# Kernel tuning notes

Measured on AMD Instinct MI355X. Metric: run time of the kernel, lower is better.

Reference implementation:

```python
import jax, jax.numpy as jnp
import numpy as np

BN_EPS = 1e-5
ATT_EPS = 1e-6


def _conv(x, w, groups=1):
    # x: [B,C,H,W], w: [O, C//groups, k, k], stride 1, SAME padding for odd k
    k = w.shape[-1]
    p = (k - 1) // 2
    return jax.lax.conv_general_dilated(
        x, w, window_strides=(1, 1), padding=[(p, p), (p, p)],
        dimension_numbers=('NCHW', 'OIHW', 'NCHW'), feature_group_count=groups)


def _bn(x, bnp):
    # bnp: [4, C] stacked (scale, bias, running_mean, running_var); eval-mode BN
    s, b, m, v = bnp[0], bnp[1], bnp[2], bnp[3]
    inv = s / jnp.sqrt(v + BN_EPS)
    return x * inv[None, :, None, None] + (b - m * inv)[None, :, None, None]


def _relu6(x):
    return jnp.clip(x, 0.0, 6.0)


def _ffn(x, fc1_w, fc1_bn, conv1_w, conv1_bn, conv2_w, conv2_bn, fc2_w, fc2_bn):
    # E_FFN: 1x1 ConvBNReLU6 -> dw5x5 ConvBNReLU6 & dw3x3 ConvBNReLU6 -> sum -> 1x1 ConvBN -> ReLU6
    C = x.shape[1]
    h = _relu6(_bn(_conv(x, fc1_w), fc1_bn))
    x1 = _relu6(_bn(_conv(h, conv1_w, groups=C), conv1_bn))
    x2 = _relu6(_bn(_conv(h, conv2_w, groups=C), conv2_bn))
    return _relu6(_bn(_conv(x1 + x2, fc2_w), fc2_bn))


def _bias(y, b):
    return y + b[None, :, None, None]


def setup_inputs() -> dict:
    key = jax.random.key(0)
    ks = jax.random.split(key, 16)
    C, M = 64, 8  # in_places, in_places // scale
    B, H, W = 4, 224, 224

    def w(k, shape, s=0.05):
        return (jax.random.normal(k, shape, dtype=jnp.float32) * s)

    def bn_params(k, c):
        k1, k2, k3, k4 = jax.random.split(k, 4)
        scale = 1.0 + 0.1 * jax.random.normal(k1, (c,), dtype=jnp.float32)
        bias = 0.1 * jax.random.normal(k2, (c,), dtype=jnp.float32)
        mean = 0.1 * jax.random.normal(k3, (c,), dtype=jnp.float32)
        var = 1.0 + 0.1 * jax.random.uniform(k4, (c,), dtype=jnp.float32)
        return jnp.stack([scale, bias, mean, var])  # [4, c]

    return {
        'x': jax.random.normal(ks[0], (B, C, H, W), dtype=jnp.float32),
        'gamma': jnp.full((1,), 0.5, dtype=jnp.float32),  # nonzero so attention branch matters
        'q_w': w(ks[1], (M, C, 1, 1)), 'q_b': w(ks[2], (M,)),
        'k_w': w(ks[3], (M, C, 1, 1)), 'k_b': w(ks[4], (M,)),
        'v_w': w(ks[5], (C, C, 1, 1)), 'v_b': w(ks[6], (C,)),
        'fc1_w': w(ks[7], (C, C, 1, 1)), 'fc1_bn': bn_params(ks[8], C),
        'conv1_w': w(ks[9], (C, 1, 5, 5)), 'conv1_bn': bn_params(ks[10], C),
        'conv2_w': w(ks[11], (C, 1, 3, 3)), 'conv2_bn': bn_params(ks[12], C),
        'fc2_w': w(ks[13], (C, C, 1, 1)), 'fc2_bn': bn_params(ks[14], C),
    }


def reference(x, gamma, q_w, q_b, k_w, k_b, v_w, v_b,
              fc1_w, fc1_bn, conv1_w, conv1_bn, conv2_w, conv2_bn, fc2_w, fc2_bn):
    B, C, H, W = x.shape
    N = H * W
    x_channel = _ffn(x, fc1_w, fc1_bn, conv1_w, conv1_bn, conv2_w, conv2_bn, fc2_w, fc2_bn)
    # softplus feature maps; Q,K: [B, m, N]
    Q = jax.nn.softplus(_bias(_conv(x, q_w), q_b).reshape(B, -1, N))
    K = jax.nn.softplus(_bias(_conv(x, k_w), k_b).reshape(B, -1, N))
    V = (_bias(_conv(x, v_w), v_b) + x_channel).reshape(B, C, N)
    Qt = jnp.swapaxes(Q, 1, 2)                              # [B, N, m]
    KV = jnp.einsum('bmn,bcn->bmc', K, V)                   # [B, m, C]
    norm = 1.0 / jnp.einsum('bnm,bm->bn', Qt, K.sum(-1) + ATT_EPS)  # [B, N]
    wv = jnp.einsum('bnm,bmc,bn->bcn', Qt, KV, norm).reshape(B, C, H, W)
    return x + gamma * wv
```

## Files before the change

kernel.cpp:

```cpp
#include <hip/hip_runtime.h>
#include <math.h>

#define B_ 4
#define C_ 64
#define M_ 8
#define H_ 224
#define W_ 224
#define N_ (H_*W_)
#define CN_ (C_*N_)
#define MN_ (M_*N_)
#define BCN_ (B_*CN_)
#define BMN_ (B_*MN_)

__device__ __forceinline__ float relu6f(float v){ return fminf(fmaxf(v,0.0f),6.0f); }
__device__ __forceinline__ float softplusf(float v){
  return v > 0.0f ? v + log1pf(expf(-v)) : log1pf(expf(v));
}

#define FMA4(A, W, X) { A.x = fmaf((W), (X).x, A.x); A.y = fmaf((W), (X).y, A.y); \
                        A.z = fmaf((W), (X).z, A.z); A.w = fmaf((W), (X).w, A.w); }

__global__ __launch_bounds__(256) void k_fc1k(const float* __restrict__ x,
                                              const float* __restrict__ w,
                                              const float* __restrict__ bn,
                                              const float* __restrict__ kw,
                                              const float* __restrict__ kb,
                                              float* __restrict__ h,
                                              float* __restrict__ Kq)
{
  __shared__ float xsl[2*1024];
  __shared__ float wl [2*512];
  __shared__ float kt [512];
  const int tid  = threadIdx.x;
  const int b    = blockIdx.x / 392;
  const int pg   = blockIdx.x % 392;
  const int pix0 = pg*128;
  const float* xb = x + (size_t)b*CN_ + pix0;

  for (int idx = tid; idx < 512; idx += 256) {
    const int c = idx >> 3, m = idx & 7;
    kt[idx] = kw[m*64 + c];
  }

  const int scp = tid >> 5;
  const int spx = (tid & 31) << 2;
  const int e0 = tid*2, e1 = tid*2+1;
  const int wc0 = e0 >> 6, wo0 = e0 & 63;
  const int wc1 = e1 >> 6, wo1 = e1 & 63;

  {
    const float4 xr = *(const float4*)(xb + (size_t)scp*N_ + spx);
    const float w0r = w[wo0*64 + wc0];
    const float w1r = w[wo1*64 + wc1];
    *(float4*)&xsl[scp*128 + spx] = xr;
    wl[e0] = w0r; wl[e1] = w1r;
  }
  __syncthreads();

  const int lane = tid & 63, wv_ = tid >> 6;
  const int och  = 2*wv_ + (lane >> 5);
  const int ocb  = och*8;
  const int px4  = (lane & 31) << 2;

  float4 ah[8];
  float4 ak = {0,0,0,0};
  #pragma unroll
  for (int i = 0; i < 8; ++i) ah[i] = make_float4(0.f,0.f,0.f,0.f);

  for (int ck = 0; ck < 8; ++ck) {
    const int cur = ck & 1, nxt = cur ^ 1;
    const float* xc = &xsl[cur*1024];
    const float* wc = &wl[cur*512];
    float4 xr; float w0r, w1r;
    if (ck < 7) {
      const int c0n = (ck+1)*8;
      xr  = *(const float4*)(xb + (size_t)(c0n + scp)*N_ + spx);
      w0r = w[wo0*64 + c0n + wc0];
      w1r = w[wo1*64 + c0n + wc1];
    }
    #pragma unroll
    for (int cp = 0; cp < 8; ++cp) {
      const float4 xv = *(const float4*)&xc[cp*128 + px4];
      const float4 w0 = *(const float4*)&wc[cp*64 + ocb];
      const float4 w1 = *(const float4*)&wc[cp*64 + ocb + 4];
      const float kvw = kt[(ck*8+cp)*8 + och];
      FMA4(ah[0], w0.x, xv); FMA4(ah[1], w0.y, xv);
      FMA4(ah[2], w0.z, xv); FMA4(ah[3], w0.w, xv);
      FMA4(ah[4], w1.x, xv); FMA4(ah[5], w1.y, xv);
      FMA4(ah[6], w1.z, xv); FMA4(ah[7], w1.w, xv);
      FMA4(ak, kvw, xv);
    }
    if (ck < 7) {
      *(float4*)&xsl[nxt*1024 + scp*128 + spx] = xr;
      wl[nxt*512 + e0] = w0r; wl[nxt*512 + e1] = w1r;
    }
    __syncthreads();
  }

  float* hb = h + (size_t)b*CN_ + pix0 + px4;
  #pragma unroll
  for (int o = 0; o < 8; ++o) {
    const int oc = ocb + o;
    const float inv  = bn[oc] / sqrtf(bn[192+oc] + 1e-5f);
    const float beta = bn[64+oc] - bn[128+oc]*inv;
    float4 o4;
    o4.x = relu6f(fmaf(ah[o].x, inv, beta));
    o4.y = relu6f(fmaf(ah[o].y, inv, beta));
    o4.z = relu6f(fmaf(ah[o].z, inv, beta));
    o4.w = relu6f(fmaf(ah[o].w, inv, beta));
    *(float4*)(hb + (size_t)oc*N_) = o4;
  }
  {
    const float kbm = kb[och];
    float4 q;
    q.x = softplusf(ak.x + kbm); q.y = softplusf(ak.y + kbm);
    q.z = softplusf(ak.z + kbm); q.w = softplusf(ak.w + kbm);
    *(float4*)(Kq + (size_t)b*MN_ + (size_t)och*N_ + pix0 + px4) = q;
  }
}

__global__ __launch_bounds__(256) void k_dw(const float* __restrict__ h,
                                            const float* __restrict__ w5,
                                            const float* __restrict__ w3,
                                            const float* __restrict__ bn1,
                                            const float* __restrict__ bn2,
                                            float* __restrict__ s)
{
  __shared__ float tile[36*37];
  const int tid = threadIdx.x;
  const int blk = blockIdx.x;
  const int t   = blk % 49;
  const int bc  = blk / 49;
  const int c   = bc & 63;
  const int tx0 = (t % 7) * 32;
  const int ty0 = (t / 7) * 32;
  const float* hb = h + (size_t)bc * N_;

  for (int idx = tid; idx < 1296; idx += 256) {
    const int ly = idx / 36, lx = idx - ly*36;
    const int gy = ty0 + ly - 2, gx = tx0 + lx - 2;
    float v = 0.0f;
    if (gy >= 0 && gy < H_ && gx >= 0 && gx < W_) v = hb[gy*W_ + gx];
    tile[ly*37 + lx] = v;
  }
  __syncthreads();

  float w5r[25], w3r[9];
  #pragma unroll
  for (int i = 0; i < 25; ++i) w5r[i] = w5[c*25 + i];
  #pragma unroll
  for (int i = 0; i < 9; ++i)  w3r[i] = w3[c*9 + i];
  const float inv1 = bn1[c] / sqrtf(bn1[192+c] + 1e-5f);
  const float bet1 = bn1[64+c] - bn1[128+c]*inv1;
  const float inv2 = bn2[c] / sqrtf(bn2[192+c] + 1e-5f);
  const float bet2 = bn2[64+c] - bn2[128+c]*inv2;

  const int ty  = tid >> 3;
  const int tx4 = (tid & 7) << 2;
  float a5[4] = {0,0,0,0}, a3[4] = {0,0,0,0};
  #pragma unroll
  for (int dy = 0; dy < 5; ++dy) {
    float r[8];
    #pragma unroll
    for (int i = 0; i < 8; ++i) r[i] = tile[(ty+dy)*37 + tx4 + i];
    #pragma unroll
    for (int dx = 0; dx < 5; ++dx) {
      const float wv = w5r[dy*5+dx];
      #pragma unroll
      for (int p = 0; p < 4; ++p) a5[p] = fmaf(wv, r[p+dx], a5[p]);
    }
    if (dy >= 1 && dy <= 3) {
      #pragma unroll
      for (int dx = 1; dx <= 3; ++dx) {
        const float wv = w3r[(dy-1)*3+(dx-1)];
        #pragma unroll
        for (int p = 0; p < 4; ++p) a3[p] = fmaf(wv, r[p+dx], a3[p]);
      }
    }
  }
  float* sb = s + (size_t)bc * N_ + (ty0+ty)*W_ + tx0 + tx4;
  float4 o4;
  o4.x = relu6f(fmaf(a5[0],inv1,bet1)) + relu6f(fmaf(a3[0],inv2,bet2));
  o4.y = relu6f(fmaf(a5[1],inv1,bet1)) + relu6f(fmaf(a3[1],inv2,bet2));
  o4.z = relu6f(fmaf(a5[2],inv1,bet1)) + relu6f(fmaf(a3[2],inv2,bet2));
  o4.w = relu6f(fmaf(a5[3],inv1,bet1)) + relu6f(fmaf(a3[3],inv2,bet2));
  *(float4*)sb = o4;
}

__global__ __launch_bounds__(256) void k_v(const float* __restrict__ x,
                                           const float* __restrict__ s,
                                           const float* __restrict__ vw,
                                           const float* __restrict__ vb,
                                           const float* __restrict__ fw,
                                           const float* __restrict__ fbn,
                                           float* __restrict__ V)
{
  __shared__ float xsl[2*1024];
  __shared__ float ssl[2*1024];
  __shared__ float wvl[2*512];
  __shared__ float wfl[2*512];
  const int tid  = threadIdx.x;
  const int b    = blockIdx.x / 392;
  const int pg   = blockIdx.x % 392;
  const int pix0 = pg*128;
  const float* xb = x + (size_t)b*CN_ + pix0;
  const float* sb = s + (size_t)b*CN_ + pix0;

  const int scp = tid >> 5;
  const int spx = (tid & 31) << 2;
  const int e0 = tid*2, e1 = tid*2+1;
  const int wc0 = e0 >> 6, wo0 = e0 & 63;
  const int wc1 = e1 >> 6, wo1 = e1 & 63;

  {
    const float4 xr = *(const float4*)(xb + (size_t)scp*N_ + spx);
    const float4 sr = *(const float4*)(sb + (size_t)scp*N_ + spx);
    const float a0 = vw[wo0*64 + wc0], a1 = vw[wo1*64 + wc1];
    const float f0 = fw[wo0*64 + wc0], f1 = fw[wo1*64 + wc1];
    *(float4*)&xsl[scp*128 + spx] = xr;
    *(float4*)&ssl[scp*128 + spx] = sr;
    wvl[e0] = a0; wvl[e1] = a1;
    wfl[e0] = f0; wfl[e1] = f1;
  }
  __syncthreads();

  const int lane = tid & 63, wv_ = tid >> 6;
  const int och  = 2*wv_ + (lane >> 5);
  const int ocb  = och*8;
  const int px4  = (lane & 31) << 2;

  float4 av[8], af[8];
  #pragma unroll
  for (int i = 0; i < 8; ++i) { av[i] = make_float4(0,0,0,0); af[i] = make_float4(0,0,0,0); }

  for (int ck = 0; ck < 8; ++ck) {
    const int cur = ck & 1, nxt = cur ^ 1;
    const float* xc = &xsl[cur*1024];
    const float* sc2 = &ssl[cur*1024];
    const float* wvc = &wvl[cur*512];
    const float* wfc = &wfl[cur*512];
    float4 xr, sr; float a0r, a1r, f0r, f1r;
    if (ck < 7) {
      const int c0n = (ck+1)*8;
      xr  = *(const float4*)(xb + (size_t)(c0n + scp)*N_ + spx);
      sr  = *(const float4*)(sb + (size_t)(c0n + scp)*N_ + spx);
      a0r = vw[wo0*64 + c0n + wc0]; a1r = vw[wo1*64 + c0n + wc1];
      f0r = fw[wo0*64 + c0n + wc0]; f1r = fw[wo1*64 + c0n + wc1];
    }
    #pragma unroll
    for (int cp = 0; cp < 8; ++cp) {
      const float4 xv = *(const float4*)&xc[cp*128 + px4];
      const float4 sv = *(const float4*)&sc2[cp*128 + px4];
      const float4 wa0 = *(const float4*)&wvc[cp*64 + ocb];
      const float4 wa1 = *(const float4*)&wvc[cp*64 + ocb + 4];
      const float4 wf0 = *(const float4*)&wfc[cp*64 + ocb];
      const float4 wf1 = *(const float4*)&wfc[cp*64 + ocb + 4];
      FMA4(av[0], wa0.x, xv); FMA4(av[1], wa0.y, xv);
      FMA4(av[2], wa0.z, xv); FMA4(av[3], wa0.w, xv);
      FMA4(av[4], wa1.x, xv); FMA4(av[5], wa1.y, xv);
      FMA4(av[6], wa1.z, xv); FMA4(av[7], wa1.w, xv);
      FMA4(af[0], wf0.x, sv); FMA4(af[1], wf0.y, sv);
      FMA4(af[2], wf0.z, sv); FMA4(af[3], wf0.w, sv);
      FMA4(af[4], wf1.x, sv); FMA4(af[5], wf1.y, sv);
      FMA4(af[6], wf1.z, sv); FMA4(af[7], wf1.w, sv);
    }
    if (ck < 7) {
      *(float4*)&xsl[nxt*1024 + scp*128 + spx] = xr;
      *(float4*)&ssl[nxt*1024 + scp*128 + spx] = sr;
      wvl[nxt*512 + e0] = a0r; wvl[nxt*512 + e1] = a1r;
      wfl[nxt*512 + e0] = f0r; wfl[nxt*512 + e1] = f1r;
    }
    __syncthreads();
  }

  float* Vb = V + (size_t)b*CN_ + pix0 + px4;
  #pragma unroll
  for (int o = 0; o < 8; ++o) {
    const int oc = ocb + o;
    const float inv  = fbn[oc] / sqrtf(fbn[192+oc] + 1e-5f);
    const float beta = fbn[64+oc] - fbn[128+oc]*inv;
    const float bias = vb[oc];
    float4 o4;
    o4.x = av[o].x + bias + relu6f(fmaf(af[o].x, inv, beta));
    o4.y = av[o].y + bias + relu6f(fmaf(af[o].y, inv, beta));
    o4.z = av[o].z + bias + relu6f(fmaf(af[o].z, inv, beta));
    o4.w = av[o].w + bias + relu6f(fmaf(af[o].w, inv, beta));
    *(float4*)(Vb + (size_t)oc*N_) = o4;
  }
}

__global__ __launch_bounds__(256) void k_kv(const float* __restrict__ V,
                                            const float* __restrict__ Kq,
                                            float* __restrict__ KV,
                                            float* __restrict__ Ksum)
{
  const int blk = blockIdx.x;
  const int b   = blk >> 7;
  const int rem = blk & 127;
  const int cg  = rem >> 4;
  const int ch  = rem & 15;
  const int tid = threadIdx.x;
  const int base = ch * 3136;
  const int end  = base + 3136;
  const float* Kb = Kq + (size_t)b*MN_;
  const float* Vb = V  + (size_t)b*CN_ + (size_t)(cg*8)*N_;

  float acc[64];
  #pragma unroll
  for (int i = 0; i < 64; ++i) acc[i] = 0.0f;
  float ks[8] = {0,0,0,0,0,0,0,0};

  for (int n = base + tid; n < end; n += 256) {
    float kv[8];
    #pragma unroll
    for (int m2 = 0; m2 < 8; ++m2) kv[m2] = Kb[m2*N_ + n];
    #pragma unroll
    for (int m2 = 0; m2 < 8; ++m2) ks[m2] += kv[m2];
    #pragma unroll
    for (int c8 = 0; c8 < 8; ++c8) {
      const float vv = Vb[c8*N_ + n];
      #pragma unroll
      for (int m2 = 0; m2 < 8; ++m2)
        acc[m2*8+c8] = fmaf(kv[m2], vv, acc[m2*8+c8]);
    }
  }
  const int lane = tid & 63;
  float mine = 0.0f;
  #pragma unroll
  for (int jj = 0; jj < 64; ++jj) {
    float v = acc[jj];
    v += __shfl_xor(v, 1);
    v += __shfl_xor(v, 2);
    v += __shfl_xor(v, 4);
    v += __shfl_xor(v, 8);
    v += __shfl_xor(v, 16);
    v += __shfl_xor(v, 32);
    if (lane == jj) mine = v;
  }
  atomicAdd(&KV[b*512 + (lane>>3)*64 + cg*8 + (lane&7)], mine);
  if (cg == 0) {
    float mk = 0.0f;
    #pragma unroll
    for (int jj = 0; jj < 8; ++jj) {
      float v = ks[jj];
      v += __shfl_xor(v, 1);
      v += __shfl_xor(v, 2);
      v += __shfl_xor(v, 4);
      v += __shfl_xor(v, 8);
      v += __shfl_xor(v, 16);
      v += __shfl_xor(v, 32);
      if (lane == jj) mk = v;
    }
    if (lane < 8) atomicAdd(&Ksum[b*8 + lane], mk);
  }
}

__global__ __launch_bounds__(256) void k_out(const float* __restrict__ x,
                                             const float* __restrict__ qw,
                                             const float* __restrict__ qb,
                                             const float* __restrict__ gamma,
                                             const float* __restrict__ KV,
                                             const float* __restrict__ Ksum,
                                             float* __restrict__ out)
{
  __shared__ float xs[64*256];
  __shared__ __align__(16) float kvt[64*8];
  __shared__ __align__(16) float wqt[64*8];
  __shared__ float ksl[8];
  const int tid = threadIdx.x;
  const int b  = blockIdx.x / 196;
  const int pg = blockIdx.x % 196;
  const int pix0 = pg*256;
  const float* xb = x + (size_t)b*CN_ + pix0;

  for (int idx = tid; idx < 512; idx += 256) {
    const int m = idx >> 6, c = idx & 63;
    kvt[c*8 + m] = KV[b*512 + idx];
    wqt[c*8 + m] = qw[idx];
  }
  if (tid < 8) ksl[tid] = Ksum[b*8 + tid] + 1e-6f;
  for (int idx = tid; idx < 4096; idx += 256) {
    const int c = idx >> 6, i = idx & 63;
    const float4 v = ((const float4*)(xb + (size_t)c*N_))[i];
    ((float4*)&xs[c*256])[i] = v;
  }
  __syncthreads();

  float q[8] = {0,0,0,0,0,0,0,0};
  #pragma unroll 8
  for (int c = 0; c < 64; ++c) {
    const float xv = xs[c*256 + tid];
    const float4 w0 = *(const float4*)&wqt[c*8];
    const float4 w1 = *(const float4*)&wqt[c*8+4];
    q[0] = fmaf(w0.x, xv, q[0]);
    q[1] = fmaf(w0.y, xv, q[1]);
    q[2] = fmaf(w0.z, xv, q[2]);
    q[3] = fmaf(w0.w, xv, q[3]);
    q[4] = fmaf(w1.x, xv, q[4]);
    q[5] = fmaf(w1.y, xv, q[5]);
    q[6] = fmaf(w1.z, xv, q[6]);
    q[7] = fmaf(w1.w, xv, q[7]);
  }
  float den = 0.0f;
  #pragma unroll
  for (int m = 0; m < 8; ++m) {
    q[m] = softplusf(q[m] + qb[m]);
    den  = fmaf(q[m], ksl[m], den);
  }
  const float sc = gamma[0] / den;

  float* ob = out + (size_t)b*CN_ + pix0 + tid;
  #pragma unroll 8
  for (int c = 0; c < 64; ++c) {
    const float4 k0 = *(const float4*)&kvt[c*8];
    const float4 k1 = *(const float4*)&kvt[c*8+4];
    float wv;
    wv = q[0]*k0.x;
    wv = fmaf(q[1], k0.y, wv);
    wv = fmaf(q[2], k0.z, wv);
    wv = fmaf(q[3], k0.w, wv);
    wv = fmaf(q[4], k1.x, wv);
    wv = fmaf(q[5], k1.y, wv);
    wv = fmaf(q[6], k1.z, wv);
    wv = fmaf(q[7], k1.w, wv);
    ob[(size_t)c*N_] = fmaf(sc, wv, xs[c*256 + tid]);
  }
}

extern "C" void kernel_launch(void* const* d_in, const int* in_sizes, int n_in,
                              void* d_out, int out_size, void* d_ws, size_t ws_size,
                              hipStream_t stream) {
  const float* x      = (const float*)d_in[0];
  const float* gamma  = (const float*)d_in[1];
  const float* q_w    = (const float*)d_in[2];
  const float* q_b    = (const float*)d_in[3];
  const float* k_w    = (const float*)d_in[4];
  const float* k_b    = (const float*)d_in[5];
  const float* v_w    = (const float*)d_in[6];
  const float* v_b    = (const float*)d_in[7];
  const float* fc1_w  = (const float*)d_in[8];
  const float* fc1_bn = (const float*)d_in[9];
  const float* c1_w   = (const float*)d_in[10];
  const float* c1_bn  = (const float*)d_in[11];
  const float* c2_w   = (const float*)d_in[12];
  const float* c2_bn  = (const float*)d_in[13];
  const float* fc2_w  = (const float*)d_in[14];
  const float* fc2_bn = (const float*)d_in[15];
  float* outp = (float*)d_out;

  float* ws   = (float*)d_ws;
  float* bufA = ws;
  float* bufS = ws + (size_t)BCN_;
  float* bufK = ws + (size_t)2*BCN_;
  float* kv   = ws + (size_t)2*BCN_ + BMN_;
  float* ksum = kv + 2048;

  hipMemsetAsync(kv, 0, (2048 + 32)*sizeof(float), stream);

  k_fc1k<<<dim3(B_*392), dim3(256), 0, stream>>>(x, fc1_w, fc1_bn, k_w, k_b, bufA, bufK);
  k_dw  <<<dim3(B_*C_*49), dim3(256), 0, stream>>>(bufA, c1_w, c2_w, c1_bn, c2_bn, bufS);
  k_v   <<<dim3(B_*392), dim3(256), 0, stream>>>(x, bufS, v_w, v_b, fc2_w, fc2_bn, bufA);
  k_kv  <<<dim3(512), dim3(256), 0, stream>>>(bufA, bufK, kv, ksum);
  k_out <<<dim3(B_*196), dim3(256), 0, stream>>>(x, q_w, q_b, gamma, kv, ksum, outp);
}
```

Measured before the change: 320.7 us.

## Fuse KV reduction into V kernel and compute Ksum in fc1 kernel

The V projection kernel now reduces its V tile against K in registers and atomically accumulates the KV matrix, so V no longer has to be written to global memory and read back by a separate KV kernel. Ksum is computed by a wave reduction plus atomic add inside the fc1/K kernel. The output kernel drops its 64KB shared-memory staging of x and reads x directly from global memory twice, which allows higher occupancy at the cost of redundant loads. The atomic count on KV rises (one per wave per block), which adds contention and makes the summation order nondeterministic.

```diff
diff --git a/kernel.cpp b/kernel.cpp
--- a/kernel.cpp
+++ b/kernel.cpp
@@ -26,7 +26,8 @@
                                               const float* __restrict__ kw,
                                               const float* __restrict__ kb,
                                               float* __restrict__ h,
-                                              float* __restrict__ Kq)
+                                              float* __restrict__ Kq,
+                                              float* __restrict__ Ksum)
 {
   __shared__ float xsl[2*1024];
   __shared__ float wl [2*512];
@@ -116,6 +117,13 @@
     q.x = softplusf(ak.x + kbm); q.y = softplusf(ak.y + kbm);
     q.z = softplusf(ak.z + kbm); q.w = softplusf(ak.w + kbm);
     *(float4*)(Kq + (size_t)b*MN_ + (size_t)och*N_ + pix0 + px4) = q;
+    float ss = (q.x + q.y) + (q.z + q.w);
+    ss += __shfl_xor(ss, 1);
+    ss += __shfl_xor(ss, 2);
+    ss += __shfl_xor(ss, 4);
+    ss += __shfl_xor(ss, 8);
+    ss += __shfl_xor(ss, 16);
+    if ((lane & 31) == 0) atomicAdd(&Ksum[b*8 + och], ss);
   }
 }
 
@@ -187,13 +195,14 @@
   *(float4*)sb = o4;
 }
 
-__global__ __launch_bounds__(256) void k_v(const float* __restrict__ x,
-                                           const float* __restrict__ s,
-                                           const float* __restrict__ vw,
-                                           const float* __restrict__ vb,
-                                           const float* __restrict__ fw,
-                                           const float* __restrict__ fbn,
-                                           float* __restrict__ V)
+__global__ __launch_bounds__(256) void k_vkv(const float* __restrict__ x,
+                                             const float* __restrict__ s,
+                                             const float* __restrict__ vw,
+                                             const float* __restrict__ vb,
+                                             const float* __restrict__ fw,
+                                             const float* __restrict__ fbn,
+                                             const float* __restrict__ Kq,
+                                             float* __restrict__ KV)
 {
   __shared__ float xsl[2*1024];
   __shared__ float ssl[2*1024];
@@ -273,85 +282,57 @@
     __syncthreads();
   }
 
-  float* Vb = V + (size_t)b*CN_ + pix0 + px4;
+  float4 v4[8];
   #pragma unroll
   for (int o = 0; o < 8; ++o) {
     const int oc = ocb + o;
     const float inv  = fbn[oc] / sqrtf(fbn[192+oc] + 1e-5f);
     const float beta = fbn[64+oc] - fbn[128+oc]*inv;
     const float bias = vb[oc];
-    float4 o4;
-    o4.x = av[o].x + bias + relu6f(fmaf(af[o].x, inv, beta));
-    o4.y = av[o].y + bias + relu6f(fmaf(af[o].y, inv, beta));
-    o4.z = av[o].z + bias + relu6f(fmaf(af[o].z, inv, beta));
-    o4.w = av[o].w + bias + relu6f(fmaf(af[o].w, inv, beta));
-    *(float4*)(Vb + (size_t)oc*N_) = o4;
-  }
-}
-
-__global__ __launch_bounds__(256) void k_kv(const float* __restrict__ V,
-                                            const float* __restrict__ Kq,
-                                            float* __restrict__ KV,
-                                            float* __restrict__ Ksum)
-{
-  const int blk = blockIdx.x;
-  const int b   = blk >> 7;
-  const int rem = blk & 127;
-  const int cg  = rem >> 4;
-  const int ch  = rem & 15;
-  const int tid = threadIdx.x;
-  const int base = ch * 3136;
-  const int end  = base + 3136;
-  const float* Kb = Kq + (size_t)b*MN_;
-  const float* Vb = V  + (size_t)b*CN_ + (size_t)(cg*8)*N_;
-
-  float acc[64];
-  #pragma unroll
-  for (int i = 0; i < 64; ++i) acc[i] = 0.0f;
-  float ks[8] = {0,0,0,0,0,0,0,0};
-
-  for (int n = base + tid; n < end; n += 256) {
-    float kv[8];
-    #pragma unroll
-    for (int m2 = 0; m2 < 8; ++m2) kv[m2] = Kb[m2*N_ + n];
-    #pragma unroll
-    for (int m2 = 0; m2 < 8; ++m2) ks[m2] += kv[m2];
-    #pragma unroll
-    for (int c8 = 0; c8 < 8; ++c8) {
-      const float vv = Vb[c8*N_ + n];
+    v4[o].x = av[o].x + bias + relu6f(fmaf(af[o].x, inv, beta));
+    v4[o].y = av[o].y + bias + relu6f(fmaf(af[o].y, inv, beta));
+    v4[o].z = av[o].z + bias + relu6f(fmaf(af[o].z, inv, beta));
+    v4[o].w = av[o].w + bias + relu6f(fmaf(af[o].w, inv, beta));
+  }
+
+  const float* Kb = Kq + (size_t)b*MN_ + pix0;
+  for (int idx = tid; idx < 1024; idx += 256)
+    xsl[idx] = Kb[(size_t)(idx >> 7)*N_ + (idx & 127)];
+  __syncthreads();
+
+  const int l31 = lane & 31;
+  #pragma unroll
+  for (int half = 0; half < 2; ++half) {
+    float p[32];
+    #pragma unroll
+    for (int m2 = 0; m2 < 4; ++m2) {
+      const float4 kv4 = *(const float4*)&xsl[(half*4+m2)*128 + px4];
       #pragma unroll
-      for (int m2 = 0; m2 < 8; ++m2)
-        acc[m2*8+c8] = fmaf(kv[m2], vv, acc[m2*8+c8]);
-    }
-  }
-  const int lane = tid & 63;
-  float mine = 0.0f;
-  #pragma unroll
-  for (int jj = 0; jj < 64; ++jj) {
-    float v = acc[jj];
-    v += __shfl_xor(v, 1);
-    v += __shfl_xor(v, 2);
-    v += __shfl_xor(v, 4);
-    v += __shfl_xor(v, 8);
-    v += __shfl_xor(v, 16);
-    v += __shfl_xor(v, 32);
-    if (lane == jj) mine = v;
-  }
-  atomicAdd(&KV[b*512 + (lane>>3)*64 + cg*8 + (lane&7)], mine);
-  if (cg == 0) {
-    float mk = 0.0f;
-    #pragma unroll
-    for (int jj = 0; jj < 8; ++jj) {
-      float v = ks[jj];
-      v += __shfl_xor(v, 1);
-      v += __shfl_xor(v, 2);
-      v += __shfl_xor(v, 4);
-      v += __shfl_xor(v, 8);
-      v += __shfl_xor(v, 16);
-      v += __shfl_xor(v, 32);
-      if (lane == jj) mk = v;
-    }
-    if (lane < 8) atomicAdd(&Ksum[b*8 + lane], mk);
+      for (int o = 0; o < 8; ++o) {
+        float t = kv4.x*v4[o].x;
+        t = fmaf(kv4.y, v4[o].y, t);
+        t = fmaf(kv4.z, v4[o].z, t);
+        t = fmaf(kv4.w, v4[o].w, t);
+        p[m2*8+o] = t;
+      }
+    }
+    int nv = 32;
+    #pragma unroll
+    for (int mask = 1; mask <= 16; mask <<= 1) {
+      nv >>= 1;
+      const bool hi = (l31 & mask) != 0;
+      #pragma unroll
+      for (int i = 0; i < nv; ++i) {
+        const float mine = hi ? p[i] : p[i+nv];
+        const float th = __shfl_xor(mine, mask);
+        p[i] = (hi ? p[i+nv] : p[i]) + th;
+      }
+    }
+    const int j = 16*(l31 & 1) + 8*((l31 >> 1) & 1) + 4*((l31 >> 2) & 1)
+                + 2*((l31 >> 3) & 1) + ((l31 >> 4) & 1);
+    const int m = half*4 + (j >> 3);
+    const int o = j & 7;
+    atomicAdd(&KV[b*512 + m*64 + ocb + o], p[0]);
   }
 }
 
@@ -363,7 +344,6 @@
                                              const float* __restrict__ Ksum,
                                              float* __restrict__ out)
 {
-  __shared__ float xs[64*256];
   __shared__ __align__(16) float kvt[64*8];
   __shared__ __align__(16) float wqt[64*8];
   __shared__ float ksl[8];
@@ -371,7 +351,7 @@
   const int b  = blockIdx.x / 196;
   const int pg = blockIdx.x % 196;
   const int pix0 = pg*256;
-  const float* xb = x + (size_t)b*CN_ + pix0;
+  const float* xb = x + (size_t)b*CN_ + pix0 + tid;
 
   for (int idx = tid; idx < 512; idx += 256) {
     const int m = idx >> 6, c = idx & 63;
@@ -379,17 +359,12 @@
     wqt[c*8 + m] = qw[idx];
   }
   if (tid < 8) ksl[tid] = Ksum[b*8 + tid] + 1e-6f;
-  for (int idx = tid; idx < 4096; idx += 256) {
-    const int c = idx >> 6, i = idx & 63;
-    const float4 v = ((const float4*)(xb + (size_t)c*N_))[i];
-    ((float4*)&xs[c*256])[i] = v;
-  }
   __syncthreads();
 
   float q[8] = {0,0,0,0,0,0,0,0};
   #pragma unroll 8
   for (int c = 0; c < 64; ++c) {
-    const float xv = xs[c*256 + tid];
+    const float xv = xb[(size_t)c*N_];
     const float4 w0 = *(const float4*)&wqt[c*8];
     const float4 w1 = *(const float4*)&wqt[c*8+4];
     q[0] = fmaf(w0.x, xv, q[0]);
@@ -423,7 +398,7 @@
     wv = fmaf(q[5], k1.y, wv);
     wv = fmaf(q[6], k1.z, wv);
     wv = fmaf(q[7], k1.w, wv);
-    ob[(size_t)c*N_] = fmaf(sc, wv, xs[c*256 + tid]);
+    ob[(size_t)c*N_] = fmaf(sc, wv, xb[(size_t)c*N_]);
   }
 }
 
@@ -457,9 +432,8 @@
 
   hipMemsetAsync(kv, 0, (2048 + 32)*sizeof(float), stream);
 
-  k_fc1k<<<dim3(B_*392), dim3(256), 0, stream>>>(x, fc1_w, fc1_bn, k_w, k_b, bufA, bufK);
+  k_fc1k<<<dim3(B_*392), dim3(256), 0, stream>>>(x, fc1_w, fc1_bn, k_w, k_b, bufA, bufK, ksum);
   k_dw  <<<dim3(B_*C_*49), dim3(256), 0, stream>>>(bufA, c1_w, c2_w, c1_bn, c2_bn, bufS);
-  k_v   <<<dim3(B_*392), dim3(256), 0, stream>>>(x, bufS, v_w, v_b, fc2_w, fc2_bn, bufA);
-  k_kv  <<<dim3(512), dim3(256), 0, stream>>>(bufA, bufK, kv, ksum);
+  k_vkv <<<dim3(B_*392), dim3(256), 0, stream>>>(x, bufS, v_w, v_b, fc2_w, fc2_bn, bufK, kv);
   k_out <<<dim3(B_*196), dim3(256), 0, stream>>>(x, q_w, q_b, gamma, kv, ksum, outp);
 }
```

Result: slower. 1.162 ms (+262.3%).
